# Optimization experiments

Hardware: AMD Instinct MI355X
Metric: run time of the kernel (lower is better)

Reference implementation:

```python
import jax, jax.numpy as jnp
import numpy as np

HEADS = 16
DIM_HEAD = 64
SCALE = DIM_HEAD ** -0.5


def setup_inputs() -> dict:
    key = jax.random.key(0)
    ks = jax.random.split(key, 7)
    b, n, m, d = 2, 2048, 2048, 1024
    inner = HEADS * DIM_HEAD  # 1024
    patch_embed = jax.random.normal(ks[0], (b, n, d), dtype=jnp.float32)
    pixel_embed = jax.random.normal(ks[1], (b, m, d), dtype=jnp.float32)
    s = 1.0 / np.sqrt(d)
    Wq = jax.random.normal(ks[2], (d, inner), dtype=jnp.float32) * s
    Wk = jax.random.normal(ks[3], (d, inner), dtype=jnp.float32) * s
    Wv = jax.random.normal(ks[4], (d, inner), dtype=jnp.float32) * s
    Wo = jax.random.normal(ks[5], (inner, d), dtype=jnp.float32) * (1.0 / np.sqrt(inner))
    bo = jax.random.normal(ks[6], (d,), dtype=jnp.float32) * 0.01
    return {"patch_embed": patch_embed, "pixel_embed": pixel_embed,
            "Wq": Wq, "Wk": Wk, "Wv": Wv, "Wo": Wo, "bo": bo}


def reference(patch_embed, pixel_embed, Wq, Wk, Wv, Wo, bo):
    b, n, _ = patch_embed.shape
    h, dh = HEADS, DIM_HEAD
    # projections
    q = patch_embed @ Wq  # [b, n, h*dh]
    k = pixel_embed @ Wk  # [b, m, h*dh]
    v = pixel_embed @ Wv  # [b, m, h*dh]
    # split heads: [b, seq, h, dh]
    q = q.reshape(b, n, h, dh)
    k = k.reshape(b, -1, h, dh)
    v = v.reshape(b, -1, h, dh)
    sim = jnp.einsum('bihd,bjhd->bhij', q, k) * SCALE  # [b, h, n, m]
    attn = jax.nn.softmax(sim, axis=-1)
    out = jnp.einsum('bhij,bjhd->bihd', attn, v)  # [b, n, h, dh]
    out = out.reshape(b, n, h * dh)
    return out @ Wo + bo  # [b, n, query_dim]
```

## Files before the change

### kernel.cpp

```cpp
#include <hip/hip_runtime.h>

#define SEQ 2048
#define DMODEL 1024
#define HEADS 16
#define DH 64
#define QSCALE 0.180336880f

typedef __attribute__((ext_vector_type(8))) short short8;
typedef __attribute__((ext_vector_type(4))) float f32x4;

__device__ __forceinline__ ushort f2bf(float x) {
  union { float f; unsigned u; } v; v.f = x;
  return (ushort)((v.u + 0x7fffu + ((v.u >> 16) & 1u)) >> 16);
}

__device__ __forceinline__ void gld16(const ushort* g, ushort* l) {
  __builtin_amdgcn_global_load_lds(
      (const __attribute__((address_space(1))) unsigned int*)g,
      (__attribute__((address_space(3))) unsigned int*)l, 16, 0, 0);
}

__device__ __forceinline__ size_t qk_idx(int bh, int s, int d) {
  return ((((size_t)bh * (SEQ / 16) + (s >> 4)) * 2 + (d >> 5)) * 64 +
          ((d >> 3) & 3) * 16 + (s & 15)) * 8 + (d & 7);
}
__device__ __forceinline__ size_t v_idx(int bh, int s, int d) {
  return ((((size_t)bh * 4 + (d >> 4)) * (SEQ / 32) + (s >> 5)) * 64 +
          ((s >> 3) & 3) * 16 + (d & 15)) * 8 + (s & 7);
}

__global__ __launch_bounds__(256) void cast_bf16(const float4* __restrict__ in0,
                                                 const float4* __restrict__ in1,
                                                 ushort4* __restrict__ out0,
                                                 ushort4* __restrict__ out1, int n4) {
  const float4* in = blockIdx.z ? in1 : in0;
  ushort4* out = blockIdx.z ? out1 : out0;
  int i = blockIdx.x * 256 + threadIdx.x;
  if (i < n4) {
    float4 f = in[i];
    out[i] = make_ushort4(f2bf(f.x), f2bf(f.y), f2bf(f.z), f2bf(f.w));
  }
}

__global__ __launch_bounds__(256) void transpose_cast(
    const float* __restrict__ W0, const float* __restrict__ W1,
    const float* __restrict__ W2, const float* __restrict__ W3,
    ushort* __restrict__ O0, ushort* __restrict__ O1,
    ushort* __restrict__ O2, ushort* __restrict__ O3) {
  __shared__ float tile[32][33];
  const int z = blockIdx.z;
  const float* in = z == 0 ? W0 : z == 1 ? W1 : z == 2 ? W2 : W3;
  ushort* out = z == 0 ? O0 : z == 1 ? O1 : z == 2 ? O2 : O3;
  const float scale = z == 0 ? QSCALE : 1.0f;
  const int tx = threadIdx.x, ty = threadIdx.y;
  const int n0 = blockIdx.x * 32, k0 = blockIdx.y * 32;
#pragma unroll
  for (int i = 0; i < 4; ++i)
    tile[ty + i * 8][tx] = in[(size_t)(k0 + ty + i * 8) * DMODEL + n0 + tx];
  __syncthreads();
#pragma unroll
  for (int i = 0; i < 4; ++i)
    out[(size_t)(n0 + ty + i * 8) * DMODEL + k0 + tx] =
        f2bf(tile[tx][ty + i * 8] * scale);
}

__global__ __launch_bounds__(256) void mfma_gemm_qkv(
    const ushort* __restrict__ pb, const ushort* __restrict__ xb,
    const ushort* __restrict__ wqt, const ushort* __restrict__ wkt,
    const ushort* __restrict__ wvt, ushort* __restrict__ qws,
    ushort* __restrict__ kws, ushort* __restrict__ vws) {
  __shared__ __align__(16) ushort As[128 * 64];
  __shared__ __align__(16) ushort Bs[128 * 64];
  const int z = blockIdx.z;
  const ushort* A = (z == 0) ? pb : xb;
  const ushort* Bt = (z == 0) ? wqt : (z == 1) ? wkt : wvt;

  const int t = threadIdx.x;
  const int w = t >> 6, lane = t & 63, ln = lane & 15, q = lane >> 4;
  const int wm = w & 1, wn = w >> 1;
  const int row0 = blockIdx.y * 128, col0 = blockIdx.x * 128;
  const int sw = ln & 7;

  f32x4 acc[4][4];
#pragma unroll
  for (int i = 0; i < 4; ++i)
#pragma unroll
    for (int j = 0; j < 4; ++j) acc[i][j] = (f32x4){0.f, 0.f, 0.f, 0.f};

  for (int k0 = 0; k0 < DMODEL; k0 += 64) {
    __syncthreads();
#pragma unroll
    for (int rep = 0; rep < 4; ++rep) {
      const int u0 = rep * 256 + w * 64;
      const int u = u0 + lane;
      const int r = u >> 3, gl = (u & 7) ^ (r & 7);
      gld16(&A[(size_t)(row0 + r) * DMODEL + k0 + gl * 8], &As[u0 * 8]);
      gld16(&Bt[(size_t)(col0 + r) * DMODEL + k0 + gl * 8], &Bs[u0 * 8]);
    }
    __syncthreads();
#pragma unroll
    for (int ks = 0; ks < 2; ++ks) {
      short8 af[4], bf[4];
#pragma unroll
      for (int rt = 0; rt < 4; ++rt)
        af[rt] = *(const short8*)&As[(wm * 64 + rt * 16 + ln) * 64 +
                                     (((ks * 4 + q) ^ sw) * 8)];
#pragma unroll
      for (int ct = 0; ct < 4; ++ct)
        bf[ct] = *(const short8*)&Bs[(wn * 64 + ct * 16 + ln) * 64 +
                                     (((ks * 4 + q) ^ sw) * 8)];
#pragma unroll
      for (int rt = 0; rt < 4; ++rt)
#pragma unroll
        for (int ct = 0; ct < 4; ++ct)
          acc[rt][ct] = __builtin_amdgcn_mfma_f32_16x16x32_bf16(af[rt], bf[ct],
                                                                acc[rt][ct], 0, 0, 0);
    }
  }

  if (z < 2) {
    ushort* dst = z == 0 ? qws : kws;
#pragma unroll
    for (int rt = 0; rt < 4; ++rt)
#pragma unroll
      for (int ct = 0; ct < 4; ++ct) {
        const int c = col0 + wn * 64 + ct * 16 + ln;
        const int h = c >> 6, d = c & 63;
#pragma unroll
        for (int reg = 0; reg < 4; ++reg) {
          const int r = row0 + wm * 64 + rt * 16 + q * 4 + reg;
          const int b = r >> 11, s = r & (SEQ - 1);
          dst[qk_idx(b * HEADS + h, s, d)] = f2bf(acc[rt][ct][reg]);
        }
      }
  } else {
#pragma unroll
    for (int rt = 0; rt < 4; ++rt)
#pragma unroll
      for (int ct = 0; ct < 4; ++ct) {
        const int c = col0 + wn * 64 + ct * 16 + ln;
        const int h = c >> 6, d = c & 63;
        const int r0 = row0 + wm * 64 + rt * 16 + q * 4;
        const int b = r0 >> 11, s0 = r0 & (SEQ - 1);
        ushort4 u4 = make_ushort4(f2bf(acc[rt][ct][0]), f2bf(acc[rt][ct][1]),
                                  f2bf(acc[rt][ct][2]), f2bf(acc[rt][ct][3]));
        *(ushort4*)&vws[v_idx(b * HEADS + h, s0, d)] = u4;
      }
  }
}

__global__ __launch_bounds__(256) void flash_mfma(const ushort* __restrict__ Qg,
                                                  const ushort* __restrict__ Kg,
                                                  const ushort* __restrict__ Vg,
                                                  ushort* __restrict__ Og) {
  __shared__ __align__(16) ushort Ps[64 * 72];

  const int t = threadIdx.x;
  const int w = t >> 6, lane = t & 63, ln = lane & 15, q = lane >> 4;
  const int qt = blockIdx.x;
  const int bh = blockIdx.y;

  const ushort* qg = Qg + (size_t)bh * SEQ * DH;
  const ushort* kg = Kg + (size_t)bh * SEQ * DH;
  const ushort* vg = Vg + (size_t)bh * DH * SEQ;

  short8 qf[2];
#pragma unroll
  for (int ks = 0; ks < 2; ++ks)
    qf[ks] = *(const short8*)&qg[((((size_t)(qt * 4 + w)) * 2 + ks) * 64 + lane) * 8];

  float l_i[4] = {0.f, 0.f, 0.f, 0.f};
  f32x4 acc_o[4];
#pragma unroll
  for (int nt = 0; nt < 4; ++nt) acc_o[nt] = (f32x4){0.f, 0.f, 0.f, 0.f};

  for (int kt = 0; kt < SEQ / 64; ++kt) {
    f32x4 accs[4];
#pragma unroll
    for (int ct = 0; ct < 4; ++ct) accs[ct] = (f32x4){0.f, 0.f, 0.f, 0.f};
#pragma unroll
    for (int ks = 0; ks < 2; ++ks) {
      short8 bfr[4];
#pragma unroll
      for (int ct = 0; ct < 4; ++ct)
        bfr[ct] = *(const short8*)&kg[((((size_t)(kt * 4 + ct)) * 2 + ks) * 64 +
                                       lane) * 8];
#pragma unroll
      for (int ct = 0; ct < 4; ++ct)
        accs[ct] = __builtin_amdgcn_mfma_f32_16x16x32_bf16(qf[ks], bfr[ct],
                                                           accs[ct], 0, 0, 0);
    }

    short8 bv[2][4];
#pragma unroll
    for (int ks2 = 0; ks2 < 2; ++ks2)
#pragma unroll
      for (int nt = 0; nt < 4; ++nt)
        bv[ks2][nt] = *(const short8*)&vg[(((size_t)nt * (SEQ / 32) + kt * 2 + ks2) *
                                           64 + lane) * 8];

#pragma unroll
    for (int ct = 0; ct < 4; ++ct)
#pragma unroll
      for (int reg = 0; reg < 4; ++reg) {
        const float p = __builtin_amdgcn_exp2f(accs[ct][reg]);
        l_i[reg] += p;
        Ps[(w * 16 + q * 4 + reg) * 72 + ct * 16 + ln] = f2bf(p);
      }

#pragma unroll
    for (int ks2 = 0; ks2 < 2; ++ks2) {
      const short8 pa = *(const short8*)&Ps[(w * 16 + ln) * 72 + ks2 * 32 + q * 8];
#pragma unroll
      for (int nt = 0; nt < 4; ++nt)
        acc_o[nt] = __builtin_amdgcn_mfma_f32_16x16x32_bf16(pa, bv[ks2][nt],
                                                            acc_o[nt], 0, 0, 0);
    }
  }

  const int b = bh >> 4, h = bh & 15;
#pragma unroll
  for (int reg = 0; reg < 4; ++reg) {
    float l = l_i[reg];
    l += __shfl_xor(l, 1, 16);
    l += __shfl_xor(l, 2, 16);
    l += __shfl_xor(l, 4, 16);
    l += __shfl_xor(l, 8, 16);
    const float inv = 1.0f / l;
    const int s = qt * 64 + w * 16 + q * 4 + reg;
#pragma unroll
    for (int nt = 0; nt < 4; ++nt)
      Og[(size_t)(b * SEQ + s) * DMODEL + h * DH + nt * 16 + ln] =
          f2bf(acc_o[nt][reg] * inv);
  }
}

__global__ __launch_bounds__(256) void mfma_gemm_out(const ushort* __restrict__ A,
                                                     const ushort* __restrict__ Bt,
                                                     const float* __restrict__ bias,
                                                     float* __restrict__ dst) {
  __shared__ __align__(16) ushort As[64 * 64];
  __shared__ __align__(16) ushort Bs[128 * 64];
  const int t = threadIdx.x;
  const int w = t >> 6, lane = t & 63, ln = lane & 15, q = lane >> 4;
  const int wm = w & 1, wn = w >> 1;
  const int row0 = blockIdx.y * 64, col0 = blockIdx.x * 128;
  const int sw = ln & 7;

  f32x4 acc[2][4];
#pragma unroll
  for (int i = 0; i < 2; ++i)
#pragma unroll
    for (int j = 0; j < 4; ++j) acc[i][j] = (f32x4){0.f, 0.f, 0.f, 0.f};

  for (int k0 = 0; k0 < DMODEL; k0 += 64) {
    __syncthreads();
#pragma unroll
    for (int rep = 0; rep < 2; ++rep) {
      const int u0 = rep * 256 + w * 64;
      const int u = u0 + lane;
      const int r = u >> 3, gl = (u & 7) ^ (r & 7);
      gld16(&A[(size_t)(row0 + r) * DMODEL + k0 + gl * 8], &As[u0 * 8]);
    }
#pragma unroll
    for (int rep = 0; rep < 4; ++rep) {
      const int u0 = rep * 256 + w * 64;
      const int u = u0 + lane;
      const int r = u >> 3, gl = (u & 7) ^ (r & 7);
      gld16(&Bt[(size_t)(col0 + r) * DMODEL + k0 + gl * 8], &Bs[u0 * 8]);
    }
    __syncthreads();
#pragma unroll
    for (int ks = 0; ks < 2; ++ks) {
      short8 af[2], bf[4];
#pragma unroll
      for (int rt = 0; rt < 2; ++rt)
        af[rt] = *(const short8*)&As[(wm * 32 + rt * 16 + ln) * 64 +
                                     (((ks * 4 + q) ^ sw) * 8)];
#pragma unroll
      for (int ct = 0; ct < 4; ++ct)
        bf[ct] = *(const short8*)&Bs[(wn * 64 + ct * 16 + ln) * 64 +
                                     (((ks * 4 + q) ^ sw) * 8)];
#pragma unroll
      for (int rt = 0; rt < 2; ++rt)
#pragma unroll
        for (int ct = 0; ct < 4; ++ct)
          acc[rt][ct] = __builtin_amdgcn_mfma_f32_16x16x32_bf16(af[rt], bf[ct],
                                                                acc[rt][ct], 0, 0, 0);
    }
  }

#pragma unroll
  for (int rt = 0; rt < 2; ++rt)
#pragma unroll
    for (int ct = 0; ct < 4; ++ct) {
      const int c = col0 + wn * 64 + ct * 16 + ln;
      const float bi = bias[c];
#pragma unroll
      for (int reg = 0; reg < 4; ++reg) {
        const int r = row0 + wm * 32 + rt * 16 + q * 4 + reg;
        dst[(size_t)r * DMODEL + c] = acc[rt][ct][reg] + bi;
      }
    }
}

extern "C" void kernel_launch(void* const* d_in, const int* in_sizes, int n_in,
                              void* d_out, int out_size, void* d_ws,
                              size_t ws_size, hipStream_t stream) {
  const float* patch = (const float*)d_in[0];
  const float* pixel = (const float*)d_in[1];
  const float* Wq = (const float*)d_in[2];
  const float* Wk = (const float*)d_in[3];
  const float* Wv = (const float*)d_in[4];
  const float* Wo = (const float*)d_in[5];
  const float* bo = (const float*)d_in[6];
  float* out = (float*)d_out;

  const size_t E = (size_t)2 * SEQ * DMODEL;
  const size_t W = (size_t)DMODEL * DMODEL;
  ushort* pb  = (ushort*)d_ws;
  ushort* xb  = pb + E;
  ushort* wqt = xb + E;
  ushort* wkt = wqt + W;
  ushort* wvt = wkt + W;
  ushort* wot = wvt + W;
  ushort* qws = wot + W;
  ushort* kws = qws + E;
  ushort* vws = kws + E;
  ushort* aws = vws + E;

  cast_bf16<<<dim3(E / 4 / 256, 1, 2), 256, 0, stream>>>(
      (const float4*)patch, (const float4*)pixel, (ushort4*)pb, (ushort4*)xb, E / 4);
  transpose_cast<<<dim3(32, 32, 4), dim3(32, 8), 0, stream>>>(
      Wq, Wk, Wv, Wo, wqt, wkt, wvt, wot);
  mfma_gemm_qkv<<<dim3(8, 32, 3), 256, 0, stream>>>(pb, xb, wqt, wkt, wvt,
                                                    qws, kws, vws);
  flash_mfma<<<dim3(32, 32), 256, 0, stream>>>(qws, kws, vws, aws);
  mfma_gemm_out<<<dim3(8, 64), 256, 0, stream>>>(aws, wot, bo, out);
}
```

Baseline: 219.7 us.

## Split attention over key range with merge pass and fuse prologue kernels

The flash attention kernel now splits the key sequence into two halves across a new grid dimension. Each half writes unnormalized fp32 partial outputs and row sums into reused workspace buffers, and a new merge kernel combines them, normalizes and casts to bf16. This doubles the number of blocks so the GPU has more parallel work. It adds 32 MB of fp32 partial-output traffic plus an extra launch. The V fragment loads are hoisted ahead of the QK MFMAs for earlier issue, and the input cast and weight transpose kernels are merged into one prologue launch.

```diff
diff --git a/kernel.cpp b/kernel.cpp
--- a/kernel.cpp
+++ b/kernel.cpp
@@ -29,30 +29,32 @@
           ((s >> 3) & 3) * 16 + (d & 15)) * 8 + (s & 7);
 }
 
-__global__ __launch_bounds__(256) void cast_bf16(const float4* __restrict__ in0,
-                                                 const float4* __restrict__ in1,
-                                                 ushort4* __restrict__ out0,
-                                                 ushort4* __restrict__ out1, int n4) {
-  const float4* in = blockIdx.z ? in1 : in0;
-  ushort4* out = blockIdx.z ? out1 : out0;
-  int i = blockIdx.x * 256 + threadIdx.x;
-  if (i < n4) {
-    float4 f = in[i];
-    out[i] = make_ushort4(f2bf(f.x), f2bf(f.y), f2bf(f.z), f2bf(f.w));
-  }
-}
-
-__global__ __launch_bounds__(256) void transpose_cast(
+__global__ __launch_bounds__(256) void prologue(
+    const float* __restrict__ patch, const float* __restrict__ pixel,
     const float* __restrict__ W0, const float* __restrict__ W1,
     const float* __restrict__ W2, const float* __restrict__ W3,
+    ushort* __restrict__ pb, ushort* __restrict__ xb,
     ushort* __restrict__ O0, ushort* __restrict__ O1,
     ushort* __restrict__ O2, ushort* __restrict__ O3) {
+  const int z = blockIdx.z;
+  const int tx = threadIdx.x, ty = threadIdx.y;
+  if (z < 2) {
+    const float4* in = (const float4*)(z ? pixel : patch);
+    ushort4* out = (ushort4*)(z ? xb : pb);
+    const int base = (blockIdx.y * 32 + blockIdx.x) * 256 + ty * 32 + tx;
+#pragma unroll
+    for (int rep = 0; rep < 4; ++rep) {
+      const int i = base + rep * 262144;
+      float4 f = in[i];
+      out[i] = make_ushort4(f2bf(f.x), f2bf(f.y), f2bf(f.z), f2bf(f.w));
+    }
+    return;
+  }
   __shared__ float tile[32][33];
-  const int z = blockIdx.z;
-  const float* in = z == 0 ? W0 : z == 1 ? W1 : z == 2 ? W2 : W3;
-  ushort* out = z == 0 ? O0 : z == 1 ? O1 : z == 2 ? O2 : O3;
-  const float scale = z == 0 ? QSCALE : 1.0f;
-  const int tx = threadIdx.x, ty = threadIdx.y;
+  const int zz = z - 2;
+  const float* in = zz == 0 ? W0 : zz == 1 ? W1 : zz == 2 ? W2 : W3;
+  ushort* out = zz == 0 ? O0 : zz == 1 ? O1 : zz == 2 ? O2 : O3;
+  const float scale = zz == 0 ? QSCALE : 1.0f;
   const int n0 = blockIdx.x * 32, k0 = blockIdx.y * 32;
 #pragma unroll
   for (int i = 0; i < 4; ++i)
@@ -149,16 +151,20 @@
   }
 }
 
-__global__ __launch_bounds__(256) void flash_mfma(const ushort* __restrict__ Qg,
-                                                  const ushort* __restrict__ Kg,
-                                                  const ushort* __restrict__ Vg,
-                                                  ushort* __restrict__ Og) {
+__global__ __launch_bounds__(256) void flash_mfma(
+    const ushort* __restrict__ Qg, const ushort* __restrict__ Kg,
+    const ushort* __restrict__ Vg, float* __restrict__ PO0,
+    float* __restrict__ PO1, float* __restrict__ L0, float* __restrict__ L1) {
   __shared__ __align__(16) ushort Ps[64 * 72];
 
   const int t = threadIdx.x;
   const int w = t >> 6, lane = t & 63, ln = lane & 15, q = lane >> 4;
   const int qt = blockIdx.x;
   const int bh = blockIdx.y;
+  const int seg = blockIdx.z;
+
+  float* __restrict__ PO = seg ? PO1 : PO0;
+  float* __restrict__ Lb = seg ? L1 : L0;
 
   const ushort* qg = Qg + (size_t)bh * SEQ * DH;
   const ushort* kg = Kg + (size_t)bh * SEQ * DH;
@@ -174,7 +180,15 @@
 #pragma unroll
   for (int nt = 0; nt < 4; ++nt) acc_o[nt] = (f32x4){0.f, 0.f, 0.f, 0.f};
 
-  for (int kt = 0; kt < SEQ / 64; ++kt) {
+  for (int kt = seg * 16; kt < seg * 16 + 16; ++kt) {
+    short8 bv[2][4];
+#pragma unroll
+    for (int ks2 = 0; ks2 < 2; ++ks2)
+#pragma unroll
+      for (int nt = 0; nt < 4; ++nt)
+        bv[ks2][nt] = *(const short8*)&vg[(((size_t)nt * (SEQ / 32) + kt * 2 + ks2) *
+                                           64 + lane) * 8];
+
     f32x4 accs[4];
 #pragma unroll
     for (int ct = 0; ct < 4; ++ct) accs[ct] = (f32x4){0.f, 0.f, 0.f, 0.f};
@@ -190,14 +204,6 @@
         accs[ct] = __builtin_amdgcn_mfma_f32_16x16x32_bf16(qf[ks], bfr[ct],
                                                            accs[ct], 0, 0, 0);
     }
-
-    short8 bv[2][4];
-#pragma unroll
-    for (int ks2 = 0; ks2 < 2; ++ks2)
-#pragma unroll
-      for (int nt = 0; nt < 4; ++nt)
-        bv[ks2][nt] = *(const short8*)&vg[(((size_t)nt * (SEQ / 32) + kt * 2 + ks2) *
-                                           64 + lane) * 8];
 
 #pragma unroll
     for (int ct = 0; ct < 4; ++ct)
@@ -218,7 +224,6 @@
     }
   }
 
-  const int b = bh >> 4, h = bh & 15;
 #pragma unroll
   for (int reg = 0; reg < 4; ++reg) {
     float l = l_i[reg];
@@ -226,13 +231,28 @@
     l += __shfl_xor(l, 2, 16);
     l += __shfl_xor(l, 4, 16);
     l += __shfl_xor(l, 8, 16);
-    const float inv = 1.0f / l;
     const int s = qt * 64 + w * 16 + q * 4 + reg;
+    if (ln == 0) Lb[bh * SEQ + s] = l;
 #pragma unroll
     for (int nt = 0; nt < 4; ++nt)
-      Og[(size_t)(b * SEQ + s) * DMODEL + h * DH + nt * 16 + ln] =
-          f2bf(acc_o[nt][reg] * inv);
-  }
+      PO[((size_t)bh * SEQ + s) * DH + nt * 16 + ln] = acc_o[nt][reg];
+  }
+}
+
+__global__ __launch_bounds__(256) void merge_reduce(
+    const float4* __restrict__ PO0, const float4* __restrict__ PO1,
+    const float* __restrict__ L0, const float* __restrict__ L1,
+    ushort* __restrict__ aws) {
+  const int i = blockIdx.x * 256 + threadIdx.x;
+  const int row = i >> 4, d4 = i & 15;
+  const int bh = row >> 11, s = row & (SEQ - 1);
+  const int b = bh >> 4, h = bh & 15;
+  const float4 a = PO0[i];
+  const float4 c = PO1[i];
+  const float inv = 1.0f / (L0[row] + L1[row]);
+  ushort4 u = make_ushort4(f2bf((a.x + c.x) * inv), f2bf((a.y + c.y) * inv),
+                           f2bf((a.z + c.z) * inv), f2bf((a.w + c.w) * inv));
+  *(ushort4*)&aws[((size_t)b * SEQ + s) * DMODEL + h * DH + d4 * 4] = u;
 }
 
 __global__ __launch_bounds__(256) void mfma_gemm_out(const ushort* __restrict__ A,
@@ -329,12 +349,17 @@
   ushort* vws = kws + E;
   ushort* aws = vws + E;
 
-  cast_bf16<<<dim3(E / 4 / 256, 1, 2), 256, 0, stream>>>(
-      (const float4*)patch, (const float4*)pixel, (ushort4*)pb, (ushort4*)xb, E / 4);
-  transpose_cast<<<dim3(32, 32, 4), dim3(32, 8), 0, stream>>>(
-      Wq, Wk, Wv, Wo, wqt, wkt, wvt, wot);
+  float* PO0 = (float*)pb;
+  float* PO1 = out;
+  float* L0 = (float*)wqt;
+  float* L1 = L0 + 32 * SEQ;
+
+  prologue<<<dim3(32, 32, 6), dim3(32, 8), 0, stream>>>(
+      patch, pixel, Wq, Wk, Wv, Wo, pb, xb, wqt, wkt, wvt, wot);
   mfma_gemm_qkv<<<dim3(8, 32, 3), 256, 0, stream>>>(pb, xb, wqt, wkt, wvt,
                                                     qws, kws, vws);
-  flash_mfma<<<dim3(32, 32), 256, 0, stream>>>(qws, kws, vws, aws);
+  flash_mfma<<<dim3(32, 32, 2), 256, 0, stream>>>(qws, kws, vws, PO0, PO1, L0, L1);
+  merge_reduce<<<dim3((32 * SEQ * DH / 4) / 256), 256, 0, stream>>>(
+      (const float4*)PO0, (const float4*)PO1, L0, L1, aws);
   mfma_gemm_out<<<dim3(8, 64), 256, 0, stream>>>(aws, wot, bo, out);
 }
```

Measured after the change: 226.1 us. +2.9%, slower.
